# Performance work log

Hardware: AMD Instinct MI355X
Metric: run time of the kernel (lower is better)

The kernel has to match this reference:

```python
import jax, jax.numpy as jnp
import numpy as np

E = 8       # num experts
D = 768     # embed_dim
H = 12      # num heads
F = 3072    # expert hidden = 4*D
TOPK = 2


def setup_inputs() -> dict:
    key = jax.random.key(0)
    ks = jax.random.split(key, 8)
    B, S = 4, 1024
    s = lambda d: 1.0 / np.sqrt(d)
    return {
        "x": jax.random.normal(ks[0], (B, S, D), jnp.float32),
        "w_qkv": jax.random.normal(ks[1], (D, 3 * D), jnp.float32) * s(D),
        "b_qkv": jnp.zeros((3 * D,), jnp.float32),
        "w_o": jax.random.normal(ks[2], (D, D), jnp.float32) * s(D),
        "b_o": jnp.zeros((D,), jnp.float32),
        "w_router": jax.random.normal(ks[3], (D, E), jnp.float32) * s(D),
        "w1": jax.random.normal(ks[4], (E, D, F), jnp.float32) * s(D),
        "b1": jnp.zeros((E, F), jnp.float32),
        "w2": jax.random.normal(ks[5], (E, F, D), jnp.float32) * s(F),
        "b2": jnp.zeros((E, D), jnp.float32),
    }


def reference(x, w_qkv, b_qkv, w_o, b_o, w_router, w1, b1, w2, b2):
    B, S, Dm = x.shape
    hd = Dm // H
    # --- multi-head self-attention ---
    qkv = x @ w_qkv + b_qkv                                  # [B,S,3D]
    q, k, v = jnp.split(qkv, 3, axis=-1)
    resh = lambda t: t.reshape(B, S, H, hd).transpose(0, 2, 1, 3)  # [B,H,S,hd]
    q, k, v = resh(q), resh(k), resh(v)
    scores = jnp.einsum('bhqd,bhkd->bhqk', q, k) / np.sqrt(hd).astype(np.float32)
    attn = jax.nn.softmax(scores, axis=-1)
    ctx = jnp.einsum('bhqk,bhkd->bhqd', attn, v)
    ctx = ctx.transpose(0, 2, 1, 3).reshape(B, S, Dm)
    y = ctx @ w_o + b_o                                      # [B,S,D]
    # --- top-k MoE feed-forward ---
    t = y.reshape(B * S, Dm)                                 # [T,D]
    logits = t @ w_router                                    # [T,E]
    probs = jax.nn.softmax(logits, axis=-1)
    topv, topi = jax.lax.top_k(probs, TOPK)                  # [T,K]
    topw = topv / jnp.sum(topv, axis=-1, keepdims=True)      # renormalized gates
    T = t.shape[0]
    wfull = jnp.zeros_like(probs).at[jnp.arange(T)[:, None], topi].set(topw)  # [T,E]
    # dense all-expert compute, weighted combine (faithful to routed math)
    h = jax.nn.gelu(jnp.einsum('td,edf->etf', t, w1) + b1[:, None, :])  # [E,T,F]
    oe = jnp.einsum('etf,efd->etd', h, w2) + b2[:, None, :]              # [E,T,D]
    out = jnp.einsum('te,etd->td', wfull, oe).reshape(B, S, Dm)
    diagnostics = probs  # router probabilities as diagnostics
    return (out, diagnostics)
```

## Files before the change

kernel.cpp:

```cpp
#include <hip/hip_runtime.h>
#include <hip/hip_bf16.h>
#include <cstdint>
#include <cmath>

#define T_TOK 4096
#define DIM   768
#define HEADS 12
#define HD    64
#define NEXP  8
#define FDIM  3072

typedef __attribute__((ext_vector_type(8))) short short8v;
typedef __attribute__((ext_vector_type(4))) float float4v;

__device__ __forceinline__ float gelu_tanh(float x) {
  float u = 0.7978845608028654f * (x + 0.044715f * x * x * x);
  return 0.5f * x * (1.0f + tanhf(u));
}

__device__ __forceinline__ short f2bf(float x) {
  __hip_bfloat16 h = __float2bfloat16(x);
  return *reinterpret_cast<short*>(&h);
}

__device__ __forceinline__ void gld16(void* lds, const void* g) {
  __builtin_amdgcn_global_load_lds(
      (__attribute__((address_space(1))) void*)(uintptr_t)g,
      (__attribute__((address_space(3))) void*)(uint32_t)(uintptr_t)lds,
      16, 0, 0);
}

template<int TBM, int TBN>
__global__ __launch_bounds__(256) void gemm_f32(
    const float* __restrict__ A, const float* __restrict__ W,
    const float* __restrict__ bias, float* __restrict__ C,
    int M, int N, int K)
{
  constexpr int MM = TBM / 16;
  constexpr int MN = TBN / 16;
  constexpr int ALOAD = TBM * 16 / 256;
  constexpr int BLOAD = TBN * 16 / 256;
  __shared__ float As[16][TBM + 4];
  __shared__ float Bs[16][TBN + 4];
  const int bm = blockIdx.y * TBM;
  const int bn = blockIdx.x * TBN;
  const int tid = threadIdx.x;
  const int tr = tid >> 4;
  const int tc = tid & 15;

  float acc[MM][MN] = {};

  for (int k0 = 0; k0 < K; k0 += 16) {
    #pragma unroll
    for (int i = 0; i < ALOAD; i++) {
      int idx = tid + i * 256;
      int m  = idx >> 4;
      int kk = idx & 15;
      As[kk][m] = A[(size_t)(bm + m) * K + k0 + kk];
    }
    #pragma unroll
    for (int i = 0; i < BLOAD; i++) {
      int idx = tid + i * 256;
      int kk = idx / TBN;
      int n  = idx % TBN;
      Bs[kk][n] = W[(size_t)(k0 + kk) * N + bn + n];
    }
    __syncthreads();
    #pragma unroll
    for (int kk = 0; kk < 16; kk++) {
      float a[MM], b[MN];
      #pragma unroll
      for (int u4 = 0; u4 < MM / 4; u4++) {
        float4 t = *(const float4*)&As[kk][tr * MM + u4 * 4];
        a[u4*4+0]=t.x; a[u4*4+1]=t.y; a[u4*4+2]=t.z; a[u4*4+3]=t.w;
      }
      #pragma unroll
      for (int v4 = 0; v4 < MN / 4; v4++) {
        float4 t = *(const float4*)&Bs[kk][tc * MN + v4 * 4];
        b[v4*4+0]=t.x; b[v4*4+1]=t.y; b[v4*4+2]=t.z; b[v4*4+3]=t.w;
      }
      #pragma unroll
      for (int u = 0; u < MM; u++)
        #pragma unroll
        for (int v = 0; v < MN; v++)
          acc[u][v] = fmaf(a[u], b[v], acc[u][v]);
    }
    __syncthreads();
  }

  #pragma unroll
  for (int u = 0; u < MM; u++) {
    int row = bm + tr * MM + u;
    #pragma unroll
    for (int v4 = 0; v4 < MN / 4; v4++) {
      int col = bn + tc * MN + v4 * 4;
      float4 o;
      o.x = acc[u][v4*4+0] + bias[col+0];
      o.y = acc[u][v4*4+1] + bias[col+1];
      o.z = acc[u][v4*4+2] + bias[col+2];
      o.w = acc[u][v4*4+3] + bias[col+3];
      *(float4*)&C[(size_t)row * N + col] = o;
    }
  }
}

__global__ __launch_bounds__(256) void transpose_bf16(
    const float* __restrict__ W, short* __restrict__ WT, int K, int N)
{
  __shared__ float t[32][33];
  const size_t mat = (size_t)K * N;
  const float* Wp = W + blockIdx.z * mat;
  short* WTp = WT + blockIdx.z * mat;
  int n0 = blockIdx.x * 32, k0 = blockIdx.y * 32;
  int tx = threadIdx.x, ty = threadIdx.y;
  #pragma unroll
  for (int i = 0; i < 4; i++)
    t[ty + i * 8][tx] = Wp[(size_t)(k0 + ty + i * 8) * N + n0 + tx];
  __syncthreads();
  #pragma unroll
  for (int i = 0; i < 4; i++)
    WTp[(size_t)(n0 + ty + i * 8) * K + k0 + tx] = f2bf(t[tx][ty + i * 8]);
}

__global__ __launch_bounds__(256) void y2bf_kernel(
    const float* __restrict__ y, short* __restrict__ ybf)
{
  int g = blockIdx.x * 256 + threadIdx.x;
  float4 v = *(const float4*)&y[(size_t)g * 4];
  short4 s = make_short4(f2bf(v.x), f2bf(v.y), f2bf(v.z), f2bf(v.w));
  *(short4*)&ybf[(size_t)g * 4] = s;
}

__global__ __launch_bounds__(256) void moe_up(
    const short* __restrict__ ybf, const short* __restrict__ WT,
    const float* __restrict__ bias, short* __restrict__ hbuf,
    const int* __restrict__ offsets, const int* __restrict__ perm)
{
  const int e = blockIdx.z;
  const int start = offsets[e];
  const int M = offsets[e + 1] - start;
  const int bm = blockIdx.y * 128;
  if (bm >= M) return;
  const int bn = blockIdx.x * 128;

  __shared__ short As[4][128][8];
  __shared__ short Bs[4][128][8];
  __shared__ int   perm_s[128];

  const int tid  = threadIdx.x;
  const int lane = tid & 63;
  const int wave = tid >> 6;
  const int wm = wave >> 1, wn = wave & 1;
  const int lr = lane & 15;
  const int kb = lane >> 4;

  const short* WTe = WT + (size_t)e * ((size_t)FDIM * DIM);
  const float* be  = bias + (size_t)e * FDIM;

  if (tid < 128) {
    int rr = bm + tid;
    perm_s[tid] = (rr < M) ? perm[start + rr] : perm[start];
  }
  __syncthreads();

  const short* asrc0 = ybf + (size_t)perm_s[lane] * DIM + wave * 8;
  const short* asrc1 = ybf + (size_t)perm_s[64 + lane] * DIM + wave * 8;
  const short* bsrc0 = WTe + (size_t)(bn + lane) * DIM + wave * 8;
  const short* bsrc1 = WTe + (size_t)(bn + 64 + lane) * DIM + wave * 8;
  short* adst0 = &As[wave][0][0];
  short* adst1 = &As[wave][64][0];
  short* bdst0 = &Bs[wave][0][0];
  short* bdst1 = &Bs[wave][64][0];

  float4v acc[4][4] = {};

  for (int k0 = 0; k0 < DIM; k0 += 32) {
    __syncthreads();
    gld16(adst0, asrc0 + k0);
    gld16(adst1, asrc1 + k0);
    gld16(bdst0, bsrc0 + k0);
    gld16(bdst1, bsrc1 + k0);
    __syncthreads();

    short8v af[4], bfv[4];
    #pragma unroll
    for (int mi = 0; mi < 4; mi++)
      af[mi] = *(const short8v*)&As[kb][wm * 64 + mi * 16 + lr][0];
    #pragma unroll
    for (int ni = 0; ni < 4; ni++)
      bfv[ni] = *(const short8v*)&Bs[kb][wn * 64 + ni * 16 + lr][0];
    #pragma unroll
    for (int mi = 0; mi < 4; mi++)
      #pragma unroll
      for (int ni = 0; ni < 4; ni++)
        acc[mi][ni] = __builtin_amdgcn_mfma_f32_16x16x32_bf16(
            af[mi], bfv[ni], acc[mi][ni], 0, 0, 0);
  }

  #pragma unroll
  for (int ni = 0; ni < 4; ni++) {
    int col = bn + wn * 64 + ni * 16 + lr;
    float b = be[col];
    #pragma unroll
    for (int mi = 0; mi < 4; mi++) {
      int lrow0 = wm * 64 + mi * 16 + kb * 4;
      #pragma unroll
      for (int r = 0; r < 4; r++) {
        int rr = bm + lrow0 + r;
        if (rr < M)
          hbuf[(size_t)(start + rr) * FDIM + col] = f2bf(gelu_tanh(acc[mi][ni][r] + b));
      }
    }
  }
}

__global__ __launch_bounds__(256) void moe_down(
    const short* __restrict__ hbuf, const short* __restrict__ WT,
    const float* __restrict__ bias, float* __restrict__ oe,
    const int* __restrict__ offsets)
{
  const int e = blockIdx.z;
  const int start = offsets[e];
  const int M = offsets[e + 1] - start;
  const int bm = blockIdx.y * 64;
  if (bm >= M) return;
  const int bn = blockIdx.x * 128;

  __shared__ short As[4][64][8];
  __shared__ short Bs[4][128][8];

  const int tid  = threadIdx.x;
  const int lane = tid & 63;
  const int wave = tid >> 6;
  const int lr   = lane & 15;
  const int kb   = lane >> 4;

  const short* WTe = WT + (size_t)e * ((size_t)DIM * FDIM);
  const float* be  = bias + (size_t)e * DIM;

  int arow = bm + lane; if (arow >= M) arow = M - 1;
  const short* asrc  = hbuf + (size_t)(start + arow) * FDIM + wave * 8;
  const short* bsrc0 = WTe + (size_t)(bn + lane) * FDIM + wave * 8;
  const short* bsrc1 = WTe + (size_t)(bn + 64 + lane) * FDIM + wave * 8;
  short* adst  = &As[wave][0][0];
  short* bdst0 = &Bs[wave][0][0];
  short* bdst1 = &Bs[wave][64][0];

  float4v acc[4][2] = {};

  for (int k0 = 0; k0 < FDIM; k0 += 32) {
    __syncthreads();
    gld16(adst,  asrc  + k0);
    gld16(bdst0, bsrc0 + k0);
    gld16(bdst1, bsrc1 + k0);
    __syncthreads();

    short8v af[4], bfv[2];
    #pragma unroll
    for (int mi = 0; mi < 4; mi++)
      af[mi] = *(const short8v*)&As[kb][mi * 16 + lr][0];
    #pragma unroll
    for (int ni = 0; ni < 2; ni++)
      bfv[ni] = *(const short8v*)&Bs[kb][wave * 32 + ni * 16 + lr][0];
    #pragma unroll
    for (int mi = 0; mi < 4; mi++)
      #pragma unroll
      for (int ni = 0; ni < 2; ni++)
        acc[mi][ni] = __builtin_amdgcn_mfma_f32_16x16x32_bf16(
            af[mi], bfv[ni], acc[mi][ni], 0, 0, 0);
  }

  #pragma unroll
  for (int ni = 0; ni < 2; ni++) {
    int col = bn + wave * 32 + ni * 16 + lr;
    float b = be[col];
    #pragma unroll
    for (int mi = 0; mi < 4; mi++) {
      #pragma unroll
      for (int r = 0; r < 4; r++) {
        int rr = bm + mi * 16 + kb * 4 + r;
        if (rr < M)
          oe[(size_t)(start + rr) * DIM + col] = acc[mi][ni][r] + b;
      }
    }
  }
}

__global__ __launch_bounds__(256) void combine_kernel(
    const float* __restrict__ oe, const int* __restrict__ ppos,
    const float* __restrict__ topg, float* __restrict__ out)
{
  int g = blockIdx.x * 256 + threadIdx.x;
  int t = g / 192;
  int c = (g - t * 192) * 4;
  int p0 = ppos[2 * t], p1 = ppos[2 * t + 1];
  float g0 = topg[2 * t], g1 = topg[2 * t + 1];
  float4 a = *(const float4*)&oe[(size_t)p0 * DIM + c];
  float4 b = *(const float4*)&oe[(size_t)p1 * DIM + c];
  float4 o;
  o.x = g0 * a.x + g1 * b.x;
  o.y = g0 * a.y + g1 * b.y;
  o.z = g0 * a.z + g1 * b.z;
  o.w = g0 * a.w + g1 * b.w;
  *(float4*)&out[(size_t)t * DIM + c] = o;
}

__global__ __launch_bounds__(512) void attn_kernel(
    const float* __restrict__ qkv, float* __restrict__ ctx)
{
  const int qt = blockIdx.x;
  const int bh = blockIdx.y;
  const int b = bh / HEADS, h = bh % HEADS;
  const float* base = qkv + (size_t)b * 1024 * (3 * DIM) + h * 64;

  __shared__ float ks[64 * 64];
  __shared__ float vs[64 * 64];
  __shared__ float lred[2][2][32];

  const int tid   = threadIdx.x;
  const int wv    = tid >> 6;
  const int qhalf = wv & 1;
  const int kq    = wv >> 1;
  const int lane  = tid & 63;
  const int grp   = lane >> 2;
  const int sub   = lane & 3;
  const int q0    = qhalf * 32 + grp * 2;
  const int dpart = sub * 16;

  const float qscale = 0.125f * 1.44269504088896f;
  float qA[16], qB[16], accA[16] = {}, accB[16] = {};
  float lA = 0.f, lB = 0.f;

  {
    const float* qpA = base + (size_t)(qt * 64 + q0) * (3 * DIM) + dpart;
    const float* qpB = qpA + 3 * DIM;
    #pragma unroll
    for (int d4 = 0; d4 < 4; d4++) {
      float4 ta = *(const float4*)(qpA + d4 * 4);
      float4 tb = *(const float4*)(qpB + d4 * 4);
      qA[d4*4+0]=ta.x*qscale; qA[d4*4+1]=ta.y*qscale; qA[d4*4+2]=ta.z*qscale; qA[d4*4+3]=ta.w*qscale;
      qB[d4*4+0]=tb.x*qscale; qB[d4*4+1]=tb.y*qscale; qB[d4*4+2]=tb.z*qscale; qB[d4*4+3]=tb.w*qscale;
    }
  }

  for (int kt = 0; kt < 16; kt++) {
    __syncthreads();
    #pragma unroll
    for (int i = 0; i < 2; i++) {
      int idx = tid + i * 512;
      int r = idx >> 4, c4 = idx & 15;
      const float* kp = base + (size_t)(kt * 64 + r) * (3 * DIM) + c4 * 4;
      *(float4*)&ks[r * 64 + c4 * 4] = *(const float4*)(kp + DIM);
      *(float4*)&vs[r * 64 + c4 * 4] = *(const float4*)(kp + 2 * DIM);
    }
    __syncthreads();

    #pragma unroll 2
    for (int jj = 0; jj < 16; jj++) {
      int j = kq * 16 + jj;
      float4 k0v = *(const float4*)&ks[j * 64 + dpart];
      float4 k1v = *(const float4*)&ks[j * 64 + dpart + 4];
      float4 k2v = *(const float4*)&ks[j * 64 + dpart + 8];
      float4 k3v = *(const float4*)&ks[j * 64 + dpart + 12];
      float kr[16] = {k0v.x,k0v.y,k0v.z,k0v.w, k1v.x,k1v.y,k1v.z,k1v.w,
                      k2v.x,k2v.y,k2v.z,k2v.w, k3v.x,k3v.y,k3v.z,k3v.w};
      float sA = 0.f, sB = 0.f;
      #pragma unroll
      for (int d = 0; d < 16; d++) {
        sA = fmaf(qA[d], kr[d], sA);
        sB = fmaf(qB[d], kr[d], sB);
      }
      sA += __shfl_xor(sA, 1);  sB += __shfl_xor(sB, 1);
      sA += __shfl_xor(sA, 2);  sB += __shfl_xor(sB, 2);
      float pA = exp2f(sA);
      float pB = exp2f(sB);
      lA += pA;  lB += pB;
      float4 v0v = *(const float4*)&vs[j * 64 + dpart];
      float4 v1v = *(const float4*)&vs[j * 64 + dpart + 4];
      float4 v2v = *(const float4*)&vs[j * 64 + dpart + 8];
      float4 v3v = *(const float4*)&vs[j * 64 + dpart + 12];
      float vr[16] = {v0v.x,v0v.y,v0v.z,v0v.w, v1v.x,v1v.y,v1v.z,v1v.w,
                      v2v.x,v2v.y,v2v.z,v2v.w, v3v.x,v3v.y,v3v.z,v3v.w};
      #pragma unroll
      for (int d = 0; d < 16; d++) {
        accA[d] = fmaf(pA, vr[d], accA[d]);
        accB[d] = fmaf(pB, vr[d], accB[d]);
      }
    }
  }

  float* regA = ks + qhalf * 2048;
  float* regB = vs + qhalf * 2048;
  const int r0 = (grp * 2) * 64 + dpart;
  const int r1 = r0 + 64;

  __syncthreads();
  if (kq == 2 || kq == 3) {
    float* buf = (kq == 2) ? regA : regB;
    #pragma unroll
    for (int d4 = 0; d4 < 4; d4++) {
      *(float4*)&buf[r0 + d4*4] =
          make_float4(accA[d4*4], accA[d4*4+1], accA[d4*4+2], accA[d4*4+3]);
      *(float4*)&buf[r1 + d4*4] =
          make_float4(accB[d4*4], accB[d4*4+1], accB[d4*4+2], accB[d4*4+3]);
    }
    if (sub == 0) {
      lred[kq - 2][qhalf][grp * 2]     = lA;
      lred[kq - 2][qhalf][grp * 2 + 1] = lB;
    }
  }
  __syncthreads();
  if (kq == 0 || kq == 1) {
    const float* buf = (kq == 0) ? regA : regB;
    #pragma unroll
    for (int d4 = 0; d4 < 4; d4++) {
      float4 a = *(const float4*)&buf[r0 + d4*4];
      float4 c = *(const float4*)&buf[r1 + d4*4];
      accA[d4*4+0] += a.x; accA[d4*4+1] += a.y; accA[d4*4+2] += a.z; accA[d4*4+3] += a.w;
      accB[d4*4+0] += c.x; accB[d4*4+1] += c.y; accB[d4*4+2] += c.z; accB[d4*4+3] += c.w;
    }
    lA += lred[kq][qhalf][grp * 2];
    lB += lred[kq][qhalf][grp * 2 + 1];
  }
  __syncthreads();
  if (kq == 1) {
    #pragma unroll
    for (int d4 = 0; d4 < 4; d4++) {
      *(float4*)&regA[r0 + d4*4] =
          make_float4(accA[d4*4], accA[d4*4+1], accA[d4*4+2], accA[d4*4+3]);
      *(float4*)&regA[r1 + d4*4] =
          make_float4(accB[d4*4], accB[d4*4+1], accB[d4*4+2], accB[d4*4+3]);
    }
    if (sub == 0) {
      lred[0][qhalf][grp * 2]     = lA;
      lred[0][qhalf][grp * 2 + 1] = lB;
    }
  }
  __syncthreads();
  if (kq == 0) {
    #pragma unroll
    for (int d4 = 0; d4 < 4; d4++) {
      float4 a = *(const float4*)&regA[r0 + d4*4];
      float4 c = *(const float4*)&regA[r1 + d4*4];
      accA[d4*4+0] += a.x; accA[d4*4+1] += a.y; accA[d4*4+2] += a.z; accA[d4*4+3] += a.w;
      accB[d4*4+0] += c.x; accB[d4*4+1] += c.y; accB[d4*4+2] += c.z; accB[d4*4+3] += c.w;
    }
    lA += lred[0][qhalf][grp * 2];
    lB += lred[0][qhalf][grp * 2 + 1];
    float invA = 1.f / lA, invB = 1.f / lB;
    float* opA = ctx + ((size_t)b * 1024 + qt * 64 + q0) * DIM + h * 64 + dpart;
    float* opB = opA + DIM;
    #pragma unroll
    for (int d4 = 0; d4 < 4; d4++) {
      float4 oa, ob;
      oa.x = accA[d4*4+0]*invA; oa.y = accA[d4*4+1]*invA;
      oa.z = accA[d4*4+2]*invA; oa.w = accA[d4*4+3]*invA;
      ob.x = accB[d4*4+0]*invB; ob.y = accB[d4*4+1]*invB;
      ob.z = accB[d4*4+2]*invB; ob.w = accB[d4*4+3]*invB;
      *(float4*)(opA + d4 * 4) = oa;
      *(float4*)(opB + d4 * 4) = ob;
    }
  }
}

__global__ __launch_bounds__(256) void router_kernel(
    const float* __restrict__ y, const float* __restrict__ wr,
    float* __restrict__ probs, int* __restrict__ topi,
    float* __restrict__ topg, int* __restrict__ counts)
{
  __shared__ float w[DIM * NEXP];
  const int tid = threadIdx.x;
  for (int i = tid; i < DIM * NEXP; i += 256) w[i] = wr[i];
  __syncthreads();

  const int t = blockIdx.x * 256 + tid;
  const float* yp = y + (size_t)t * DIM;
  float logit[8] = {};
  for (int d = 0; d < DIM; d++) {
    float xv = yp[d];
    #pragma unroll
    for (int e = 0; e < 8; e++) logit[e] = fmaf(xv, w[d * 8 + e], logit[e]);
  }
  float mx = logit[0];
  #pragma unroll
  for (int e = 1; e < 8; e++) mx = fmaxf(mx, logit[e]);
  float p[8], sum = 0.f;
  #pragma unroll
  for (int e = 0; e < 8; e++) { p[e] = __expf(logit[e] - mx); sum += p[e]; }
  float inv = 1.f / sum;
  #pragma unroll
  for (int e = 0; e < 8; e++) { p[e] *= inv; probs[(size_t)t * 8 + e] = p[e]; }

  int i0 = 0;
  #pragma unroll
  for (int e = 1; e < 8; e++) if (p[e] > p[i0]) i0 = e;
  int i1 = (i0 == 0) ? 1 : 0;
  #pragma unroll
  for (int e = 0; e < 8; e++) if (e != i0 && p[e] > p[i1]) i1 = e;
  float g = p[i0] + p[i1];
  topi[2 * t] = i0;  topi[2 * t + 1] = i1;
  topg[2 * t] = p[i0] / g;  topg[2 * t + 1] = p[i1] / g;
  atomicAdd(&counts[i0], 1);
  atomicAdd(&counts[i1], 1);
}

__global__ void init_meta(int* counts) {
  if (threadIdx.x < 8) counts[threadIdx.x] = 0;
}

__global__ void scan_kernel(const int* __restrict__ counts,
                            int* __restrict__ offsets, int* __restrict__ cursors) {
  if (threadIdx.x == 0) {
    int s = 0;
    for (int e = 0; e < 8; e++) { offsets[e] = s; cursors[e] = s; s += counts[e]; }
    offsets[8] = s;
  }
}

__global__ __launch_bounds__(256) void scatter_kernel(
    const int* __restrict__ topi, int* __restrict__ cursors,
    int* __restrict__ perm, int* __restrict__ ppos)
{
  const int t = blockIdx.x * 256 + threadIdx.x;
  #pragma unroll
  for (int s = 0; s < 2; s++) {
    int e = topi[2 * t + s];
    int pos = atomicAdd(&cursors[e], 1);
    perm[pos] = t;
    ppos[2 * t + s] = pos;
  }
}

extern "C" void kernel_launch(void* const* d_in, const int* in_sizes, int n_in,
                              void* d_out, int out_size, void* d_ws, size_t ws_size,
                              hipStream_t stream) {
  const float* x        = (const float*)d_in[0];
  const float* w_qkv    = (const float*)d_in[1];
  const float* b_qkv    = (const float*)d_in[2];
  const float* w_o      = (const float*)d_in[3];
  const float* b_o      = (const float*)d_in[4];
  const float* w_router = (const float*)d_in[5];
  const float* w1       = (const float*)d_in[6];
  const float* b1       = (const float*)d_in[7];
  const float* w2       = (const float*)d_in[8];
  const float* b2       = (const float*)d_in[9];

  float* out   = (float*)d_out;
  float* probs = out + (size_t)T_TOK * DIM;

  char* ws = (char*)d_ws;
  float* qkv  = (float*)ws;
  short* hbuf = (short*)ws;
  short* wT   = (short*)(ws + 50331648);
  float* ctx  = (float*)(ws + 88080384);
  short* ybf  = (short*)(ws + 88080384);
  float* oe   = (float*)(ws + 88080384);
  float* y    = (float*)(ws + 100663296);
  char*  meta = ws + 113246208;
  int*   counts  = (int*)meta;
  int*   cursors = counts + 8;
  int*   offsets = cursors + 8;
  int*   topi    = offsets + 16;
  float* topg    = (float*)(topi + 8192);
  int*   perm    = (int*)(topg + 8192);
  int*   ppos    = perm + 8192;

  init_meta<<<1, 64, 0, stream>>>(counts);

  gemm_f32<128, 64><<<dim3((3 * DIM) / 64, T_TOK / 128), 256, 0, stream>>>(
      x, w_qkv, b_qkv, qkv, T_TOK, 3 * DIM, DIM);

  attn_kernel<<<dim3(16, 48), 512, 0, stream>>>(qkv, ctx);

  gemm_f32<64, 64><<<dim3(DIM / 64, T_TOK / 64), 256, 0, stream>>>(
      ctx, w_o, b_o, y, T_TOK, DIM, DIM);

  router_kernel<<<16, 256, 0, stream>>>(y, w_router, probs, topi, topg, counts);
  scan_kernel<<<1, 64, 0, stream>>>(counts, offsets, cursors);
  scatter_kernel<<<16, 256, 0, stream>>>(topi, cursors, perm, ppos);

  y2bf_kernel<<<(T_TOK * DIM / 4) / 256, 256, 0, stream>>>(y, ybf);

  transpose_bf16<<<dim3(FDIM / 32, DIM / 32, NEXP), dim3(32, 8), 0, stream>>>(
      w1, wT, DIM, FDIM);
  moe_up<<<dim3(FDIM / 128, T_TOK / 128, NEXP), 256, 0, stream>>>(
      ybf, wT, b1, hbuf, offsets, perm);

  transpose_bf16<<<dim3(DIM / 32, FDIM / 32, NEXP), dim3(32, 8), 0, stream>>>(
      w2, wT, FDIM, DIM);
  moe_down<<<dim3(DIM / 128, T_TOK / 64, NEXP), 256, 0, stream>>>(
      hbuf, wT, b2, oe, offsets);

  combine_kernel<<<(T_TOK * DIM / 4) / 256, 256, 0, stream>>>(oe, ppos, topg, out);
}
```

Baseline: 1.080 ms.

## Double-buffer MoE GEMM tiles, vectorize fp32 GEMM loads, restructure attention inner loop

The MoE up and down GEMMs now double-buffer their LDS tiles. The next k-slice is issued via global_load_lds before the MFMAs on the current slice, and one barrier per iteration replaces two. The fp32 GEMM loads A and W tiles with float4 global loads instead of scalar loads. The attention kernel keeps Q and the accumulators in float4 registers and fully unrolls the key loop. The goals are to hide global load latency, cut barrier and memory instruction counts, and improve register allocation, at the cost of doubled LDS and possible register pressure from the unroll.

```diff
diff --git a/kernel.cpp b/kernel.cpp
--- a/kernel.cpp
+++ b/kernel.cpp
@@ -30,6 +30,15 @@
       16, 0, 0);
 }
 
+#define DOT4(s, q, k) \
+  s = fmaf((q).x, (k).x, s); s = fmaf((q).y, (k).y, s); \
+  s = fmaf((q).z, (k).z, s); s = fmaf((q).w, (k).w, s)
+#define FMA4(a, p, v) \
+  (a).x = fmaf(p, (v).x, (a).x); (a).y = fmaf(p, (v).y, (a).y); \
+  (a).z = fmaf(p, (v).z, (a).z); (a).w = fmaf(p, (v).w, (a).w)
+#define ADD4(a, v) \
+  (a).x += (v).x; (a).y += (v).y; (a).z += (v).z; (a).w += (v).w
+
 template<int TBM, int TBN>
 __global__ __launch_bounds__(256) void gemm_f32(
     const float* __restrict__ A, const float* __restrict__ W,
@@ -38,8 +47,8 @@
 {
   constexpr int MM = TBM / 16;
   constexpr int MN = TBN / 16;
-  constexpr int ALOAD = TBM * 16 / 256;
-  constexpr int BLOAD = TBN * 16 / 256;
+  constexpr int AL4 = TBM / 64;
+  constexpr int BL4 = TBN / 64;
   __shared__ float As[16][TBM + 4];
   __shared__ float Bs[16][TBN + 4];
   const int bm = blockIdx.y * TBM;
@@ -52,18 +61,21 @@
 
   for (int k0 = 0; k0 < K; k0 += 16) {
     #pragma unroll
-    for (int i = 0; i < ALOAD; i++) {
-      int idx = tid + i * 256;
-      int m  = idx >> 4;
-      int kk = idx & 15;
-      As[kk][m] = A[(size_t)(bm + m) * K + k0 + kk];
-    }
-    #pragma unroll
-    for (int i = 0; i < BLOAD; i++) {
-      int idx = tid + i * 256;
-      int kk = idx / TBN;
-      int n  = idx % TBN;
-      Bs[kk][n] = W[(size_t)(k0 + kk) * N + bn + n];
+    for (int i = 0; i < AL4; i++) {
+      int fidx = tid + i * 256;
+      int row = fidx >> 2, c4 = fidx & 3;
+      float4 v = *(const float4*)&A[(size_t)(bm + row) * K + k0 + c4 * 4];
+      As[c4 * 4 + 0][row] = v.x;
+      As[c4 * 4 + 1][row] = v.y;
+      As[c4 * 4 + 2][row] = v.z;
+      As[c4 * 4 + 3][row] = v.w;
+    }
+    #pragma unroll
+    for (int i = 0; i < BL4; i++) {
+      int fidx = tid + i * 256;
+      int kk = fidx / (TBN / 4), n4 = fidx % (TBN / 4);
+      *(float4*)&Bs[kk][n4 * 4] =
+          *(const float4*)&W[(size_t)(k0 + kk) * N + bn + n4 * 4];
     }
     __syncthreads();
     #pragma unroll
@@ -143,8 +155,8 @@
   if (bm >= M) return;
   const int bn = blockIdx.x * 128;
 
-  __shared__ short As[4][128][8];
-  __shared__ short Bs[4][128][8];
+  __shared__ short As[2][4][128][8];
+  __shared__ short Bs[2][4][128][8];
   __shared__ int   perm_s[128];
 
   const int tid  = threadIdx.x;
@@ -167,34 +179,39 @@
   const short* asrc1 = ybf + (size_t)perm_s[64 + lane] * DIM + wave * 8;
   const short* bsrc0 = WTe + (size_t)(bn + lane) * DIM + wave * 8;
   const short* bsrc1 = WTe + (size_t)(bn + 64 + lane) * DIM + wave * 8;
-  short* adst0 = &As[wave][0][0];
-  short* adst1 = &As[wave][64][0];
-  short* bdst0 = &Bs[wave][0][0];
-  short* bdst1 = &Bs[wave][64][0];
+
+  gld16(&As[0][wave][0][0],  asrc0);
+  gld16(&As[0][wave][64][0], asrc1);
+  gld16(&Bs[0][wave][0][0],  bsrc0);
+  gld16(&Bs[0][wave][64][0], bsrc1);
+  __syncthreads();
 
   float4v acc[4][4] = {};
-
-  for (int k0 = 0; k0 < DIM; k0 += 32) {
-    __syncthreads();
-    gld16(adst0, asrc0 + k0);
-    gld16(adst1, asrc1 + k0);
-    gld16(bdst0, bsrc0 + k0);
-    gld16(bdst1, bsrc1 + k0);
-    __syncthreads();
-
+  int cur = 0;
+
+  for (int t = 0; t < DIM / 32; t++) {
+    if (t < DIM / 32 - 1) {
+      int k1 = (t + 1) * 32;
+      gld16(&As[cur ^ 1][wave][0][0],  asrc0 + k1);
+      gld16(&As[cur ^ 1][wave][64][0], asrc1 + k1);
+      gld16(&Bs[cur ^ 1][wave][0][0],  bsrc0 + k1);
+      gld16(&Bs[cur ^ 1][wave][64][0], bsrc1 + k1);
+    }
     short8v af[4], bfv[4];
     #pragma unroll
     for (int mi = 0; mi < 4; mi++)
-      af[mi] = *(const short8v*)&As[kb][wm * 64 + mi * 16 + lr][0];
+      af[mi] = *(const short8v*)&As[cur][kb][wm * 64 + mi * 16 + lr][0];
     #pragma unroll
     for (int ni = 0; ni < 4; ni++)
-      bfv[ni] = *(const short8v*)&Bs[kb][wn * 64 + ni * 16 + lr][0];
+      bfv[ni] = *(const short8v*)&Bs[cur][kb][wn * 64 + ni * 16 + lr][0];
     #pragma unroll
     for (int mi = 0; mi < 4; mi++)
       #pragma unroll
       for (int ni = 0; ni < 4; ni++)
         acc[mi][ni] = __builtin_amdgcn_mfma_f32_16x16x32_bf16(
             af[mi], bfv[ni], acc[mi][ni], 0, 0, 0);
+    __syncthreads();
+    cur ^= 1;
   }
 
   #pragma unroll
@@ -226,8 +243,8 @@
   if (bm >= M) return;
   const int bn = blockIdx.x * 128;
 
-  __shared__ short As[4][64][8];
-  __shared__ short Bs[4][128][8];
+  __shared__ short As[2][4][64][8];
+  __shared__ short Bs[2][4][128][8];
 
   const int tid  = threadIdx.x;
   const int lane = tid & 63;
@@ -242,32 +259,37 @@
   const short* asrc  = hbuf + (size_t)(start + arow) * FDIM + wave * 8;
   const short* bsrc0 = WTe + (size_t)(bn + lane) * FDIM + wave * 8;
   const short* bsrc1 = WTe + (size_t)(bn + 64 + lane) * FDIM + wave * 8;
-  short* adst  = &As[wave][0][0];
-  short* bdst0 = &Bs[wave][0][0];
-  short* bdst1 = &Bs[wave][64][0];
+
+  gld16(&As[0][wave][0][0],  asrc);
+  gld16(&Bs[0][wave][0][0],  bsrc0);
+  gld16(&Bs[0][wave][64][0], bsrc1);
+  __syncthreads();
 
   float4v acc[4][2] = {};
-
-  for (int k0 = 0; k0 < FDIM; k0 += 32) {
-    __syncthreads();
-    gld16(adst,  asrc  + k0);
-    gld16(bdst0, bsrc0 + k0);
-    gld16(bdst1, bsrc1 + k0);
-    __syncthreads();
-
+  int cur = 0;
+
+  for (int t = 0; t < FDIM / 32; t++) {
+    if (t < FDIM / 32 - 1) {
+      int k1 = (t + 1) * 32;
+      gld16(&As[cur ^ 1][wave][0][0],  asrc  + k1);
+      gld16(&Bs[cur ^ 1][wave][0][0],  bsrc0 + k1);
+      gld16(&Bs[cur ^ 1][wave][64][0], bsrc1 + k1);
+    }
     short8v af[4], bfv[2];
     #pragma unroll
     for (int mi = 0; mi < 4; mi++)
-      af[mi] = *(const short8v*)&As[kb][mi * 16 + lr][0];
+      af[mi] = *(const short8v*)&As[cur][kb][mi * 16 + lr][0];
     #pragma unroll
     for (int ni = 0; ni < 2; ni++)
-      bfv[ni] = *(const short8v*)&Bs[kb][wave * 32 + ni * 16 + lr][0];
+      bfv[ni] = *(const short8v*)&Bs[cur][kb][wave * 32 + ni * 16 + lr][0];
     #pragma unroll
     for (int mi = 0; mi < 4; mi++)
       #pragma unroll
       for (int ni = 0; ni < 2; ni++)
         acc[mi][ni] = __builtin_amdgcn_mfma_f32_16x16x32_bf16(
             af[mi], bfv[ni], acc[mi][ni], 0, 0, 0);
+    __syncthreads();
+    cur ^= 1;
   }
 
   #pragma unroll
@@ -328,20 +350,26 @@
   const int dpart = sub * 16;
 
   const float qscale = 0.125f * 1.44269504088896f;
-  float qA[16], qB[16], accA[16] = {}, accB[16] = {};
+  float4 qA0, qA1, qA2, qA3, qB0, qB1, qB2, qB3;
+  float4 aA0 = {0,0,0,0}, aA1 = {0,0,0,0}, aA2 = {0,0,0,0}, aA3 = {0,0,0,0};
+  float4 aB0 = {0,0,0,0}, aB1 = {0,0,0,0}, aB2 = {0,0,0,0}, aB3 = {0,0,0,0};
   float lA = 0.f, lB = 0.f;
 
   {
     const float* qpA = base + (size_t)(qt * 64 + q0) * (3 * DIM) + dpart;
     const float* qpB = qpA + 3 * DIM;
-    #pragma unroll
-    for (int d4 = 0; d4 < 4; d4++) {
-      float4 ta = *(const float4*)(qpA + d4 * 4);
-      float4 tb = *(const float4*)(qpB + d4 * 4);
-      qA[d4*4+0]=ta.x*qscale; qA[d4*4+1]=ta.y*qscale; qA[d4*4+2]=ta.z*qscale; qA[d4*4+3]=ta.w*qscale;
-      qB[d4*4+0]=tb.x*qscale; qB[d4*4+1]=tb.y*qscale; qB[d4*4+2]=tb.z*qscale; qB[d4*4+3]=tb.w*qscale;
-    }
-  }
+    float4 t;
+    t = *(const float4*)(qpA);      qA0 = make_float4(t.x*qscale, t.y*qscale, t.z*qscale, t.w*qscale);
+    t = *(const float4*)(qpA + 4);  qA1 = make_float4(t.x*qscale, t.y*qscale, t.z*qscale, t.w*qscale);
+    t = *(const float4*)(qpA + 8);  qA2 = make_float4(t.x*qscale, t.y*qscale, t.z*qscale, t.w*qscale);
+    t = *(const float4*)(qpA + 12); qA3 = make_float4(t.x*qscale, t.y*qscale, t.z*qscale, t.w*qscale);
+    t = *(const float4*)(qpB);      qB0 = make_float4(t.x*qscale, t.y*qscale, t.z*qscale, t.w*qscale);
+    t = *(const float4*)(qpB + 4);  qB1 = make_float4(t.x*qscale, t.y*qscale, t.z*qscale, t.w*qscale);
+    t = *(const float4*)(qpB + 8);  qB2 = make_float4(t.x*qscale, t.y*qscale, t.z*qscale, t.w*qscale);
+    t = *(const float4*)(qpB + 12); qB3 = make_float4(t.x*qscale, t.y*qscale, t.z*qscale, t.w*qscale);
+  }
+
+  const int kbase = kq * 16 * 64 + dpart;
 
   for (int kt = 0; kt < 16; kt++) {
     __syncthreads();
@@ -355,37 +383,28 @@
     }
     __syncthreads();
 
-    #pragma unroll 2
+    #pragma unroll
     for (int jj = 0; jj < 16; jj++) {
-      int j = kq * 16 + jj;
-      float4 k0v = *(const float4*)&ks[j * 64 + dpart];
-      float4 k1v = *(const float4*)&ks[j * 64 + dpart + 4];
-      float4 k2v = *(const float4*)&ks[j * 64 + dpart + 8];
-      float4 k3v = *(const float4*)&ks[j * 64 + dpart + 12];
-      float kr[16] = {k0v.x,k0v.y,k0v.z,k0v.w, k1v.x,k1v.y,k1v.z,k1v.w,
-                      k2v.x,k2v.y,k2v.z,k2v.w, k3v.x,k3v.y,k3v.z,k3v.w};
+      const float* kp = &ks[kbase + jj * 64];
+      float4 k0v = *(const float4*)(kp);
+      float4 k1v = *(const float4*)(kp + 4);
+      float4 k2v = *(const float4*)(kp + 8);
+      float4 k3v = *(const float4*)(kp + 12);
       float sA = 0.f, sB = 0.f;
-      #pragma unroll
-      for (int d = 0; d < 16; d++) {
-        sA = fmaf(qA[d], kr[d], sA);
-        sB = fmaf(qB[d], kr[d], sB);
-      }
+      DOT4(sA, qA0, k0v); DOT4(sA, qA1, k1v); DOT4(sA, qA2, k2v); DOT4(sA, qA3, k3v);
+      DOT4(sB, qB0, k0v); DOT4(sB, qB1, k1v); DOT4(sB, qB2, k2v); DOT4(sB, qB3, k3v);
       sA += __shfl_xor(sA, 1);  sB += __shfl_xor(sB, 1);
       sA += __shfl_xor(sA, 2);  sB += __shfl_xor(sB, 2);
       float pA = exp2f(sA);
       float pB = exp2f(sB);
       lA += pA;  lB += pB;
-      float4 v0v = *(const float4*)&vs[j * 64 + dpart];
-      float4 v1v = *(const float4*)&vs[j * 64 + dpart + 4];
-      float4 v2v = *(const float4*)&vs[j * 64 + dpart + 8];
-      float4 v3v = *(const float4*)&vs[j * 64 + dpart + 12];
-      float vr[16] = {v0v.x,v0v.y,v0v.z,v0v.w, v1v.x,v1v.y,v1v.z,v1v.w,
-                      v2v.x,v2v.y,v2v.z,v2v.w, v3v.x,v3v.y,v3v.z,v3v.w};
-      #pragma unroll
-      for (int d = 0; d < 16; d++) {
-        accA[d] = fmaf(pA, vr[d], accA[d]);
-        accB[d] = fmaf(pB, vr[d], accB[d]);
-      }
+      const float* vp = &vs[kbase + jj * 64];
+      float4 v0v = *(const float4*)(vp);
+      float4 v1v = *(const float4*)(vp + 4);
+      float4 v2v = *(const float4*)(vp + 8);
+      float4 v3v = *(const float4*)(vp + 12);
+      FMA4(aA0, pA, v0v); FMA4(aA1, pA, v1v); FMA4(aA2, pA, v2v); FMA4(aA3, pA, v3v);
+      FMA4(aB0, pB, v0v); FMA4(aB1, pB, v1v); FMA4(aB2, pB, v2v); FMA4(aB3, pB, v3v);
     }
   }
 
@@ -397,13 +416,14 @@
   __syncthreads();
   if (kq == 2 || kq == 3) {
     float* buf = (kq == 2) ? regA : regB;
-    #pragma unroll
-    for (int d4 = 0; d4 < 4; d4++) {
-      *(float4*)&buf[r0 + d4*4] =
-          make_float4(accA[d4*4], accA[d4*4+1], accA[d4*4+2], accA[d4*4+3]);
-      *(float4*)&buf[r1 + d4*4] =
-          make_float4(accB[d4*4], accB[d4*4+1], accB[d4*4+2], accB[d4*4+3]);
-    }
+    *(float4*)&buf[r0]      = aA0;
+    *(float4*)&buf[r0 + 4]  = aA1;
+    *(float4*)&buf[r0 + 8]  = aA2;
+    *(float4*)&buf[r0 + 12] = aA3;
+    *(float4*)&buf[r1]      = aB0;
+    *(float4*)&buf[r1 + 4]  = aB1;
+    *(float4*)&buf[r1 + 8]  = aB2;
+    *(float4*)&buf[r1 + 12] = aB3;
     if (sub == 0) {
       lred[kq - 2][qhalf][grp * 2]     = lA;
       lred[kq - 2][qhalf][grp * 2 + 1] = lB;
@@ -412,25 +432,28 @@
   __syncthreads();
   if (kq == 0 || kq == 1) {
     const float* buf = (kq == 0) ? regA : regB;
-    #pragma unroll
-    for (int d4 = 0; d4 < 4; d4++) {
-      float4 a = *(const float4*)&buf[r0 + d4*4];
-      float4 c = *(const float4*)&buf[r1 + d4*4];
-      accA[d4*4+0] += a.x; accA[d4*4+1] += a.y; accA[d4*4+2] += a.z; accA[d4*4+3] += a.w;
-      accB[d4*4+0] += c.x; accB[d4*4+1] += c.y; accB[d4*4+2] += c.z; accB[d4*4+3] += c.w;
-    }
+    float4 t;
+    t = *(const float4*)&buf[r0];      ADD4(aA0, t);
+    t = *(const float4*)&buf[r0 + 4];  ADD4(aA1, t);
+    t = *(const float4*)&buf[r0 + 8];  ADD4(aA2, t);
+    t = *(const float4*)&buf[r0 + 12]; ADD4(aA3, t);
+    t = *(const float4*)&buf[r1];      ADD4(aB0, t);
+    t = *(const float4*)&buf[r1 + 4];  ADD4(aB1, t);
+    t = *(const float4*)&buf[r1 + 8];  ADD4(aB2, t);
+    t = *(const float4*)&buf[r1 + 12]; ADD4(aB3, t);
     lA += lred[kq][qhalf][grp * 2];
     lB += lred[kq][qhalf][grp * 2 + 1];
   }
   __syncthreads();
   if (kq == 1) {
-    #pragma unroll
-    for (int d4 = 0; d4 < 4; d4++) {
-      *(float4*)&regA[r0 + d4*4] =
-          make_float4(accA[d4*4], accA[d4*4+1], accA[d4*4+2], accA[d4*4+3]);
-      *(float4*)&regA[r1 + d4*4] =
-          make_float4(accB[d4*4], accB[d4*4+1], accB[d4*4+2], accB[d4*4+3]);
-    }
+    *(float4*)&regA[r0]      = aA0;
+    *(float4*)&regA[r0 + 4]  = aA1;
+    *(float4*)&regA[r0 + 8]  = aA2;
+    *(float4*)&regA[r0 + 12] = aA3;
+    *(float4*)&regA[r1]      = aB0;
+    *(float4*)&regA[r1 + 4]  = aB1;
+    *(float4*)&regA[r1 + 8]  = aB2;
+    *(float4*)&regA[r1 + 12] = aB3;
     if (sub == 0) {
       lred[0][qhalf][grp * 2]     = lA;
       lred[0][qhalf][grp * 2 + 1] = lB;
@@ -438,28 +461,28 @@
   }
   __syncthreads();
   if (kq == 0) {
-    #pragma unroll
-    for (int d4 = 0; d4 < 4; d4++) {
-      float4 a = *(const float4*)&regA[r0 + d4*4];
-      float4 c = *(const float4*)&regA[r1 + d4*4];
-      accA[d4*4+0] += a.x; accA[d4*4+1] += a.y; accA[d4*4+2] += a.z; accA[d4*4+3] += a.w;
-      accB[d4*4+0] += c.x; accB[d4*4+1] += c.y; accB[d4*4+2] += c.z; accB[d4*4+3] += c.w;
-    }
+    float4 t;
+    t = *(const float4*)&regA[r0];      ADD4(aA0, t);
+    t = *(const float4*)&regA[r0 + 4];  ADD4(aA1, t);
+    t = *(const float4*)&regA[r0 + 8];  ADD4(aA2, t);
+    t = *(const float4*)&regA[r0 + 12]; ADD4(aA3, t);
+    t = *(const float4*)&regA[r1];      ADD4(aB0, t);
+    t = *(const float4*)&regA[r1 + 4];  ADD4(aB1, t);
+    t = *(const float4*)&regA[r1 + 8];  ADD4(aB2, t);
+    t = *(const float4*)&regA[r1 + 12]; ADD4(aB3, t);
     lA += lred[0][qhalf][grp * 2];
     lB += lred[0][qhalf][grp * 2 + 1];
     float invA = 1.f / lA, invB = 1.f / lB;
     float* opA = ctx + ((size_t)b * 1024 + qt * 64 + q0) * DIM + h * 64 + dpart;
     float* opB = opA + DIM;
-    #pragma unroll
-    for (int d4 = 0; d4 < 4; d4++) {
-      float4 oa, ob;
-      oa.x = accA[d4*4+0]*invA; oa.y = accA[d4*4+1]*invA;
-      oa.z = accA[d4*4+2]*invA; oa.w = accA[d4*4+3]*invA;
-      ob.x = accB[d4*4+0]*invB; ob.y = accB[d4*4+1]*invB;
-      ob.z = accB[d4*4+2]*invB; ob.w = accB[d4*4+3]*invB;
-      *(float4*)(opA + d4 * 4) = oa;
-      *(float4*)(opB + d4 * 4) = ob;
-    }
+    *(float4*)(opA)      = make_float4(aA0.x*invA, aA0.y*invA, aA0.z*invA, aA0.w*invA);
+    *(float4*)(opA + 4)  = make_float4(aA1.x*invA, aA1.y*invA, aA1.z*invA, aA1.w*invA);
+    *(float4*)(opA + 8)  = make_float4(aA2.x*invA, aA2.y*invA, aA2.z*invA, aA2.w*invA);
+    *(float4*)(opA + 12) = make_float4(aA3.x*invA, aA3.y*invA, aA3.z*invA, aA3.w*invA);
+    *(float4*)(opB)      = make_float4(aB0.x*invB, aB0.y*invB, aB0.z*invB, aB0.w*invB);
+    *(float4*)(opB + 4)  = make_float4(aB1.x*invB, aB1.y*invB, aB1.z*invB, aB1.w*invB);
+    *(float4*)(opB + 8)  = make_float4(aB2.x*invB, aB2.y*invB, aB2.z*invB, aB2.w*invB);
+    *(float4*)(opB + 12) = make_float4(aB3.x*invB, aB3.y*invB, aB3.z*invB, aB3.w*invB);
   }
 }
 
```

Result: slower. 1.145 ms (+6.1%).
